# Performance work log

Hardware: AMD Instinct MI355X
Metric: run time of the kernel (lower is better)

The kernel has to match this reference:

```python
import jax, jax.numpy as jnp
from jax import lax
import numpy as np
from jax.scipy.special import logsumexp

B, T, K = 64, 4096, 32

def setup_inputs() -> dict:
    key = jax.random.key(0)
    k1, k2, k3 = jax.random.split(key, 3)
    return {
        "emission_logp": jax.random.normal(k1, (B, T, K), dtype=jnp.float32),
        "log_pi": jax.random.normal(k2, (K,), dtype=jnp.float32),
        "log_A": jax.random.normal(k3, (K, K), dtype=jnp.float32),
    }

def reference(emission_logp, log_pi, log_A):
    b, t, k = emission_logp.shape
    lp = jax.nn.log_softmax(log_pi)            # [K]
    lA = jax.nn.log_softmax(log_A, axis=1)     # [K,K]
    em = jnp.swapaxes(emission_logp, 0, 1)     # [T,B,K] time-major for scan

    # forward recursion: alpha_t = logsumexp_i(alpha_{t-1,i} + A_{i,j}) + em_t
    a0 = lp[None, :] + em[0]                   # [B,K]
    def fstep(a_prev, e_t):
        a_new = logsumexp(a_prev[:, :, None] + lA[None, :, :], axis=1) + e_t
        return a_new, a_new
    _, alphas = lax.scan(fstep, a0, em[1:])
    alpha = jnp.concatenate([a0[None], alphas], axis=0)  # [T,B,K]

    # backward recursion: beta_t = logsumexp_j(beta_{t+1,j} + A_{i,j} + em_{t+1,j})
    bT = jnp.zeros((b, k), dtype=emission_logp.dtype)
    def bstep(b_next, e_next):
        b_new = logsumexp(b_next[:, None, :] + lA[None, :, :] + e_next[:, None, :], axis=2)
        return b_new, b_new
    _, betas = lax.scan(bstep, bT, em[1:], reverse=True)
    beta = jnp.concatenate([betas, bT[None]], axis=0)    # [T,B,K]

    log_gamma = alpha + beta
    log_gamma = log_gamma - logsumexp(log_gamma, axis=-1, keepdims=True)
    return jnp.swapaxes(log_gamma, 0, 1)       # [B,T,K]
```

## Files before the change

kernel.cpp:

```cpp
#include <hip/hip_runtime.h>

#define B_ 64
#define T_ 4096
#define K_ 32
#define C_ 128
#define L_ 32
#define W_ 32
#define NPH 16

typedef float f32x16 __attribute__((ext_vector_type(16)));
typedef float f32x4v __attribute__((ext_vector_type(4)));
typedef short s16x8 __attribute__((ext_vector_type(8)));

union W4 { unsigned u[4]; short s[8]; s16x8 v; };

__device__ __forceinline__ unsigned cvt_pk_bf16(float lo, float hi) {
  unsigned r;
  asm("v_cvt_pk_bf16_f32 %0, %1, %2" : "=v"(r) : "v"(lo), "v"(hi));
  return r;
}
__device__ __forceinline__ short f2bf(float x) {
  unsigned u = __float_as_uint(x);
  return (short)((u + 0x7FFFu + ((u >> 16) & 1u)) >> 16);
}
__device__ __forceinline__ float wmax32(float v) {
#pragma unroll
  for (int k = 16; k >= 1; k >>= 1) v = fmaxf(v, __shfl_xor(v, k, 32));
  return v;
}
__device__ __forceinline__ float wsum32(float v) {
#pragma unroll
  for (int k = 16; k >= 1; k >>= 1) v += __shfl_xor(v, k, 32);
  return v;
}

__global__ __launch_bounds__(256) void pet_kernel(const float* __restrict__ em,
                                                  const float* __restrict__ log_pi,
                                                  const float* __restrict__ log_A,
                                                  float* __restrict__ eA,
                                                  float* __restrict__ lp,
                                                  unsigned* __restrict__ peP) {
  const int bid = (int)blockIdx.x;
  const int tid = (int)threadIdx.x;
  if (bid >= T_) {
    const int i0 = tid >> 5, j = tid & 31;
#pragma unroll
    for (int rr = 0; rr < 4; ++rr) {
      int i = i0 + 8 * rr;
      float a = log_A[i * K_ + j];
      float m = wmax32(a);
      float e = __expf(a - m);
      float S = wsum32(e);
      eA[i * K_ + j] = e / S;
    }
    if (i0 == 0) {
      float v = log_pi[j];
      float m2 = wmax32(v);
      float ee = __expf(v - m2);
      float SS = wsum32(ee);
      lp[j] = v - m2 - __logf(SS);
    }
    return;
  }
  const int t = ((bid & 7) << 9) + (bid >> 3);
  __shared__ float tile[K_][B_];
  const int b = tid >> 2, kq = tid & 3;
  const float* p = em + (size_t)b * (T_ * K_) + (size_t)t * K_ + kq * 8;
  f32x4v v0 = *(const f32x4v*)p;
  f32x4v v1 = *(const f32x4v*)(p + 4);
#pragma unroll
  for (int q = 0; q < 4; ++q) tile[kq * 8 + q][b] = __expf(v0[q]);
#pragma unroll
  for (int q = 0; q < 4; ++q) tile[kq * 8 + 4 + q][b] = __expf(v1[q]);
  __syncthreads();
  unsigned* ob = peP + (size_t)t * 1024;
#pragma unroll
  for (int rr = 0; rr < 4; ++rr) {
    int Wd = tid + 256 * rr;
    int col = Wd & 63, wq = (Wd >> 6) & 7, hh = Wd >> 9;
    int s0 = 2 * (wq & 1) + 8 * (wq >> 1) + 4 * hh;
    ob[Wd] = cvt_pk_bf16(tile[s0][col], tile[s0 + 1][col]);
  }
}

__global__ __launch_bounds__(256) void hmm_kernel(const unsigned* __restrict__ peP,
                                                  const float* __restrict__ eA,
                                                  const float* __restrict__ lp,
                                                  float* __restrict__ out) {
  __shared__ __align__(16) unsigned aw[L_ * 512];
  __shared__ __align__(16) unsigned bw[L_ * 512];
  __shared__ __align__(16) unsigned prF[2 * 4 * 512];
  __shared__ __align__(16) unsigned prB[2 * 4 * 512];

  const int bid = (int)blockIdx.x;
  const int c = ((bid & 7) << 4) + ((bid >> 3) & 15);
  const int g = bid >> 7;
  const int tid = (int)threadIdx.x;
  const int wv = tid >> 6;
  const int l = tid & 63;
  const int h = l >> 5;
  const int m = l & 31;
  const int t0 = c * L_;

  const int dsgn = (wv == 3) ? -1 : 1;
  const int tbase = (wv == 3) ? (t0 + L_ - 1 + W_) : (t0 - W_);
  const unsigned* gsrc = peP + (g << 5) + ((l >> 3) << 6) + ((l & 7) << 2);
  uint4 pr[2][8];

  W4 A1u, A2u, B1u, B2u;
  unsigned rg[8];
  f32x16 zk;
#pragma unroll
  for (int r = 0; r < 16; ++r) zk[r] = 0.0f;

  if (wv < 2) {
#pragma unroll
    for (int r = 0; r < 8; ++r) {
      const int k1 = (r & 3) + 8 * (r >> 2) + 4 * h;
      const int k2 = k1 + 16;
      float a1 = (wv == 0) ? eA[k1 * K_ + m] : eA[m * K_ + k1];
      float a2 = (wv == 0) ? eA[k2 * K_ + m] : eA[m * K_ + k2];
      A1u.s[r] = f2bf(a1);
      A2u.s[r] = f2bf(a2);
    }
#pragma unroll
    for (int q = 0; q < 4; ++q) { B1u.u[q] = 0x3F803F80u; B2u.u[q] = 0x3F803F80u; }
  } else {
    unsigned* ring = (wv == 2) ? prF : prB;
#pragma unroll
    for (int i = 0; i < 8; ++i) {
      int tv = tbase + dsgn * (i >> 1);
      tv = tv < 0 ? 0 : (tv > T_ - 1 ? T_ - 1 : tv);
      pr[0][i] = *(const uint4*)(gsrc + (size_t)tv * 1024 + ((i & 1) << 9));
    }
#pragma unroll
    for (int i = 0; i < 8; ++i)
      *(uint4*)&ring[((i >> 1)) * 512 + ((i & 1) << 8) + 4 * l] = pr[0][i];
#pragma unroll
    for (int i = 0; i < 8; ++i) {
      int tv = tbase + dsgn * (4 + (i >> 1));
      tv = tv < 0 ? 0 : (tv > T_ - 1 ? T_ - 1 : tv);
      pr[1][i] = *(const uint4*)(gsrc + (size_t)tv * 1024 + ((i & 1) << 9));
    }
  }
  __syncthreads();

#define FSTEP(P, U)                                                            \
  {                                                                            \
    const int sg = 4 * (P) + (U);                                              \
    _Pragma("unroll") for (int w = 0; w < 8; ++w)                              \
      rg[w] = prF[(((P) & 1) * 4 + (U)) * 512 + h * 256 + w * 32 + m];         \
    f32x16 acc = __builtin_amdgcn_mfma_f32_32x32x16_bf16(A1u.v, B1u.v, zk, 0, 0, 0); \
    acc = __builtin_amdgcn_mfma_f32_32x32x16_bf16(A2u.v, B2u.v, acc, 0, 0, 0); \
    if (sg == 32 && c == 0) {                                                  \
      _Pragma("unroll") for (int r = 0; r < 16; ++r)                           \
        acc[r] = __expf(lp[(r & 3) + 8 * (r >> 2) + 4 * h]);                   \
    }                                                                          \
    float al[16];                                                              \
    _Pragma("unroll") for (int w = 0; w < 8; ++w) {                            \
      al[2 * w]     = acc[2 * w]     * __uint_as_float(rg[w] << 16);           \
      al[2 * w + 1] = acc[2 * w + 1] * __uint_as_float(rg[w] & 0xFFFF0000u);   \
    }                                                                          \
    if ((sg & 7) == 7) {                                                       \
      float a0 = __shfl(al[0], m, 64);                                         \
      float rs = __builtin_amdgcn_rcpf(a0);                                    \
      _Pragma("unroll") for (int r = 0; r < 16; ++r) al[r] *= rs;              \
    }                                                                          \
    W4 nB1, nB2;                                                               \
    _Pragma("unroll") for (int q = 0; q < 4; ++q) {                            \
      nB1.u[q] = cvt_pk_bf16(al[2 * q], al[2 * q + 1]);                        \
      nB2.u[q] = cvt_pk_bf16(al[8 + 2 * q], al[8 + 2 * q + 1]);                \
    }                                                                          \
    if (sg >= 32) {                                                            \
      unsigned* bp = &aw[(sg - 32) * 512 + ((h << 5) + m) * 8];                \
      *(uint4*)bp = *(uint4*)nB1.u;                                            \
      *(uint4*)(bp + 4) = *(uint4*)nB2.u;                                      \
    }                                                                          \
    B1u = nB1; B2u = nB2;                                                      \
  }

#define BSTEP(P, U)                                                            \
  {                                                                            \
    const int sg = 4 * (P) + (U);                                              \
    _Pragma("unroll") for (int w = 0; w < 8; ++w)                              \
      rg[w] = prB[(((P) & 1) * 4 + (U)) * 512 + h * 256 + w * 32 + m];         \
    f32x16 acc = __builtin_amdgcn_mfma_f32_32x32x16_bf16(A1u.v, B1u.v, zk, 0, 0, 0); \
    acc = __builtin_amdgcn_mfma_f32_32x32x16_bf16(A2u.v, B2u.v, acc, 0, 0, 0); \
    if (sg == 32 && c == C_ - 1) {                                             \
      _Pragma("unroll") for (int r = 0; r < 16; ++r) acc[r] = 1.0f;            \
    }                                                                          \
    if (sg >= 32) {                                                            \
      W4 s1, s2;                                                               \
      _Pragma("unroll") for (int q = 0; q < 4; ++q) {                          \
        s1.u[q] = cvt_pk_bf16(acc[2 * q], acc[2 * q + 1]);                     \
        s2.u[q] = cvt_pk_bf16(acc[8 + 2 * q], acc[8 + 2 * q + 1]);             \
      }                                                                        \
      unsigned* bp = &bw[(63 - sg) * 512 + ((h << 5) + m) * 8];                \
      *(uint4*)bp = *(uint4*)s1.u;                                             \
      *(uint4*)(bp + 4) = *(uint4*)s2.u;                                       \
    }                                                                          \
    float al[16];                                                              \
    _Pragma("unroll") for (int w = 0; w < 8; ++w) {                            \
      al[2 * w]     = acc[2 * w]     * __uint_as_float(rg[w] << 16);           \
      al[2 * w + 1] = acc[2 * w + 1] * __uint_as_float(rg[w] & 0xFFFF0000u);   \
    }                                                                          \
    if ((sg & 7) == 7) {                                                       \
      float a0 = __shfl(al[0], m, 64);                                         \
      float rs = __builtin_amdgcn_rcpf(a0);                                    \
      _Pragma("unroll") for (int r = 0; r < 16; ++r) al[r] *= rs;              \
    }                                                                          \
    W4 nB1, nB2;                                                               \
    _Pragma("unroll") for (int q = 0; q < 4; ++q) {                            \
      nB1.u[q] = cvt_pk_bf16(al[2 * q], al[2 * q + 1]);                        \
      nB2.u[q] = cvt_pk_bf16(al[8 + 2 * q], al[8 + 2 * q + 1]);                \
    }                                                                          \
    B1u = nB1; B2u = nB2;                                                      \
  }

#pragma unroll
  for (int p = 0; p < NPH; ++p) {
    if (wv == 0) {
      FSTEP(p, 0) FSTEP(p, 1) FSTEP(p, 2) FSTEP(p, 3)
    } else if (wv == 1) {
      BSTEP(p, 0) BSTEP(p, 1) BSTEP(p, 2) BSTEP(p, 3)
    } else {
      unsigned* ring = (wv == 2) ? prF : prB;
      if (p < NPH - 1) {
#pragma unroll
        for (int i = 0; i < 8; ++i)
          *(uint4*)&ring[(((p + 1) & 1) * 4 + (i >> 1)) * 512 + ((i & 1) << 8) + 4 * l] =
              pr[(p + 1) & 1][i];
      }
      if (p < NPH - 2) {
#pragma unroll
        for (int i = 0; i < 8; ++i) {
          int tv = tbase + dsgn * (4 * (p + 2) + (i >> 1));
          tv = tv < 0 ? 0 : (tv > T_ - 1 ? T_ - 1 : tv);
          pr[p & 1][i] = *(const uint4*)(gsrc + (size_t)tv * 1024 + ((i & 1) << 9));
        }
      }
    }
    __syncthreads();
  }

  {
#pragma unroll
    for (int rr = 0; rr < 8; ++rr) {
      const int row = wv * 8 + rr;
      const unsigned* ap = &aw[row * 512 + ((h << 5) + m) * 8];
      const unsigned* bp = &bw[row * 512 + ((h << 5) + m) * 8];
      uint4 a1 = *(const uint4*)ap, a2 = *(const uint4*)(ap + 4);
      uint4 b1 = *(const uint4*)bp, b2 = *(const uint4*)(bp + 4);
      float gg[16];
#pragma unroll
      for (int q = 0; q < 4; ++q) {
        unsigned ua = ((const unsigned*)&a1)[q], ub = ((const unsigned*)&b1)[q];
        gg[2 * q]     = __uint_as_float(ua << 16) * __uint_as_float(ub << 16);
        gg[2 * q + 1] = __uint_as_float(ua & 0xFFFF0000u) * __uint_as_float(ub & 0xFFFF0000u);
        unsigned va = ((const unsigned*)&a2)[q], vb = ((const unsigned*)&b2)[q];
        gg[8 + 2 * q]     = __uint_as_float(va << 16) * __uint_as_float(vb << 16);
        gg[8 + 2 * q + 1] = __uint_as_float(va & 0xFFFF0000u) * __uint_as_float(vb & 0xFFFF0000u);
      }
      float s = 0.0f;
#pragma unroll
      for (int r = 0; r < 16; ++r) s += gg[r];
      s += __shfl_xor(s, 32, 64);
      const float ls = __log2f(s);
      float* po = out + (size_t)((g << 5) + m) * (T_ * K_) + (size_t)(t0 + row) * K_;
#pragma unroll
      for (int w = 0; w < 8; ++w) {
        const int k0 = 2 * (w & 1) + 8 * (w >> 1) + 4 * h;
        float2 v;
        v.x = (__log2f(gg[2 * w]) - ls) * 0.6931471805599453f;
        v.y = (__log2f(gg[2 * w + 1]) - ls) * 0.6931471805599453f;
        *(float2*)(po + k0) = v;
      }
    }
  }
}

extern "C" void kernel_launch(void* const* d_in, const int* in_sizes, int n_in,
                              void* d_out, int out_size, void* d_ws, size_t ws_size,
                              hipStream_t stream) {
  const float* em = (const float*)d_in[0];
  const float* log_pi = (const float*)d_in[1];
  const float* log_A = (const float*)d_in[2];
  float* out = (float*)d_out;

  float* eA = (float*)d_ws;
  float* lp = eA + K_ * K_;
  unsigned* peP = (unsigned*)((char*)d_ws + 8192);

  pet_kernel<<<T_ + 1, 256, 0, stream>>>(em, log_pi, log_A, eA, lp, peP);
  hmm_kernel<<<2 * C_, 256, 0, stream>>>(peP, eA, lp, out);
}
```

Baseline: 41.79 us.

## Use shorter chunks with more blocks and per-lane register prefetch rings

Splits the time axis into 512 chunks of 8 steps with a 28-step warmup, in place of 128 chunks of 32 steps with a 32-step warmup. Each block now has two waves and no dedicated loader waves. Each compute wave prefetches its emission columns four steps ahead into registers, which removes the per-phase __syncthreads and the LDS staging ring. The shared-memory layout of the alpha and beta buffers changes to scalar strided stores. This gives more parallelism and a shorter serial chain per block, but the warmup-to-output ratio rises from 1:1 to 3.5:1, so redundant work grows and loads use narrower scalar accesses.

```diff
diff --git a/kernel.cpp b/kernel.cpp
--- a/kernel.cpp
+++ b/kernel.cpp
@@ -3,10 +3,11 @@
 #define B_ 64
 #define T_ 4096
 #define K_ 32
-#define C_ 128
-#define L_ 32
-#define W_ 32
-#define NPH 16
+#define C_ 512
+#define L_ 8
+#define W_ 28
+#define PFD 4
+#define NS (W_ + L_)
 
 typedef float f32x16 __attribute__((ext_vector_type(16)));
 typedef float f32x4v __attribute__((ext_vector_type(4)));
@@ -83,76 +84,67 @@
   }
 }
 
-__global__ __launch_bounds__(256) void hmm_kernel(const unsigned* __restrict__ peP,
-                                                  const float* __restrict__ eA,
-                                                  const float* __restrict__ lp,
-                                                  float* __restrict__ out) {
+__global__ __launch_bounds__(128) void hmm2_kernel(const unsigned* __restrict__ peP,
+                                                   const float* __restrict__ eA,
+                                                   const float* __restrict__ lp,
+                                                   float* __restrict__ out) {
   __shared__ __align__(16) unsigned aw[L_ * 512];
   __shared__ __align__(16) unsigned bw[L_ * 512];
-  __shared__ __align__(16) unsigned prF[2 * 4 * 512];
-  __shared__ __align__(16) unsigned prB[2 * 4 * 512];
-
   const int bid = (int)blockIdx.x;
-  const int c = ((bid & 7) << 4) + ((bid >> 3) & 15);
-  const int g = bid >> 7;
+  const int c = ((bid & 7) << 6) + ((bid >> 3) & 63);
+  const int g = bid >> 9;
   const int tid = (int)threadIdx.x;
   const int wv = tid >> 6;
   const int l = tid & 63;
   const int h = l >> 5;
   const int m = l & 31;
   const int t0 = c * L_;
-
-  const int dsgn = (wv == 3) ? -1 : 1;
-  const int tbase = (wv == 3) ? (t0 + L_ - 1 + W_) : (t0 - W_);
-  const unsigned* gsrc = peP + (g << 5) + ((l >> 3) << 6) + ((l & 7) << 2);
-  uint4 pr[2][8];
+  const unsigned* pB = peP + (h << 9) + (g << 5) + m;
+
+  f32x16 zk;
+#pragma unroll
+  for (int r = 0; r < 16; ++r) zk[r] = 0.0f;
 
   W4 A1u, A2u, B1u, B2u;
-  unsigned rg[8];
-  f32x16 zk;
-#pragma unroll
-  for (int r = 0; r < 16; ++r) zk[r] = 0.0f;
-
-  if (wv < 2) {
-#pragma unroll
-    for (int r = 0; r < 8; ++r) {
-      const int k1 = (r & 3) + 8 * (r >> 2) + 4 * h;
-      const int k2 = k1 + 16;
-      float a1 = (wv == 0) ? eA[k1 * K_ + m] : eA[m * K_ + k1];
-      float a2 = (wv == 0) ? eA[k2 * K_ + m] : eA[m * K_ + k2];
-      A1u.s[r] = f2bf(a1);
-      A2u.s[r] = f2bf(a2);
-    }
-#pragma unroll
-    for (int q = 0; q < 4; ++q) { B1u.u[q] = 0x3F803F80u; B2u.u[q] = 0x3F803F80u; }
+#pragma unroll
+  for (int r = 0; r < 8; ++r) {
+    const int k1 = (r & 3) + 8 * (r >> 2) + 4 * h;
+    const int k2 = k1 + 16;
+    float a1 = (wv == 0) ? eA[k1 * K_ + m] : eA[m * K_ + k1];
+    float a2 = (wv == 0) ? eA[k2 * K_ + m] : eA[m * K_ + k2];
+    A1u.s[r] = f2bf(a1);
+    A2u.s[r] = f2bf(a2);
+  }
+#pragma unroll
+  for (int q = 0; q < 4; ++q) { B1u.u[q] = 0x3F803F80u; B2u.u[q] = 0x3F803F80u; }
+
+  unsigned ring[PFD][8];
+  if (wv == 0) {
+#pragma unroll
+    for (int u = 0; u < PFD; ++u) {
+      int tt = t0 - W_ + u; if (tt < 0) tt = 0;
+      const unsigned* pp = pB + (size_t)tt * 1024;
+#pragma unroll
+      for (int w = 0; w < 8; ++w) ring[u][w] = pp[w * 64];
+    }
   } else {
-    unsigned* ring = (wv == 2) ? prF : prB;
-#pragma unroll
-    for (int i = 0; i < 8; ++i) {
-      int tv = tbase + dsgn * (i >> 1);
-      tv = tv < 0 ? 0 : (tv > T_ - 1 ? T_ - 1 : tv);
-      pr[0][i] = *(const uint4*)(gsrc + (size_t)tv * 1024 + ((i & 1) << 9));
-    }
-#pragma unroll
-    for (int i = 0; i < 8; ++i)
-      *(uint4*)&ring[((i >> 1)) * 512 + ((i & 1) << 8) + 4 * l] = pr[0][i];
-#pragma unroll
-    for (int i = 0; i < 8; ++i) {
-      int tv = tbase + dsgn * (4 + (i >> 1));
-      tv = tv < 0 ? 0 : (tv > T_ - 1 ? T_ - 1 : tv);
-      pr[1][i] = *(const uint4*)(gsrc + (size_t)tv * 1024 + ((i & 1) << 9));
-    }
-  }
-  __syncthreads();
-
-#define FSTEP(P, U)                                                            \
+#pragma unroll
+    for (int u = 0; u < PFD; ++u) {
+      int tt = t0 + L_ - 1 + W_ - u; if (tt > T_ - 1) tt = T_ - 1;
+      const unsigned* pp = pB + (size_t)tt * 1024;
+#pragma unroll
+      for (int w = 0; w < 8; ++w) ring[u][w] = pp[w * 64];
+    }
+  }
+
+#define FSTEP(S)                                                               \
   {                                                                            \
-    const int sg = 4 * (P) + (U);                                              \
-    _Pragma("unroll") for (int w = 0; w < 8; ++w)                              \
-      rg[w] = prF[(((P) & 1) * 4 + (U)) * 512 + h * 256 + w * 32 + m];         \
+    const int t = t0 + ((S) - W_);                                             \
+    unsigned rg[8];                                                            \
+    _Pragma("unroll") for (int w = 0; w < 8; ++w) rg[w] = ring[(S) & 3][w];    \
     f32x16 acc = __builtin_amdgcn_mfma_f32_32x32x16_bf16(A1u.v, B1u.v, zk, 0, 0, 0); \
     acc = __builtin_amdgcn_mfma_f32_32x32x16_bf16(A2u.v, B2u.v, acc, 0, 0, 0); \
-    if (sg == 32 && c == 0) {                                                  \
+    if (t == 0) {             \
       _Pragma("unroll") for (int r = 0; r < 16; ++r)                           \
         acc[r] = __expf(lp[(r & 3) + 8 * (r >> 2) + 4 * h]);                   \
     }                                                                          \
@@ -161,7 +153,10 @@
       al[2 * w]     = acc[2 * w]     * __uint_as_float(rg[w] << 16);           \
       al[2 * w + 1] = acc[2 * w + 1] * __uint_as_float(rg[w] & 0xFFFF0000u);   \
     }                                                                          \
-    if ((sg & 7) == 7) {                                                       \
+    { int tn = t + PFD; if (tn < 0) tn = 0; if (tn > T_ - 1) tn = T_ - 1;      \
+      const unsigned* pp = pB + (size_t)tn * 1024;                             \
+      _Pragma("unroll") for (int w = 0; w < 8; ++w) ring[(S) & 3][w] = pp[w * 64]; } \
+    if (((S) & 7) == 7) {                                                      \
       float a0 = __shfl(al[0], m, 64);                                         \
       float rs = __builtin_amdgcn_rcpf(a0);                                    \
       _Pragma("unroll") for (int r = 0; r < 16; ++r) al[r] *= rs;              \
@@ -171,40 +166,47 @@
       nB1.u[q] = cvt_pk_bf16(al[2 * q], al[2 * q + 1]);                        \
       nB2.u[q] = cvt_pk_bf16(al[8 + 2 * q], al[8 + 2 * q + 1]);                \
     }                                                                          \
-    if (sg >= 32) {                                                            \
-      unsigned* bp = &aw[(sg - 32) * 512 + ((h << 5) + m) * 8];                \
-      *(uint4*)bp = *(uint4*)nB1.u;                                            \
-      *(uint4*)(bp + 4) = *(uint4*)nB2.u;                                      \
+    if ((S) >= W_) {                                                           \
+      unsigned* bp = &aw[(((S) - W_) << 9) + h * 32 + m];                      \
+      _Pragma("unroll") for (int q = 0; q < 4; ++q) {                          \
+        bp[q * 64] = nB1.u[q];                                                 \
+        bp[(4 + q) * 64] = nB2.u[q];                                           \
+      }                                                                        \
     }                                                                          \
     B1u = nB1; B2u = nB2;                                                      \
   }
 
-#define BSTEP(P, U)                                                            \
+#define BSTEP(S)                                                               \
   {                                                                            \
-    const int sg = 4 * (P) + (U);                                              \
-    _Pragma("unroll") for (int w = 0; w < 8; ++w)                              \
-      rg[w] = prB[(((P) & 1) * 4 + (U)) * 512 + h * 256 + w * 32 + m];         \
+    const int t = t0 + (L_ - 1 + W_ - (S));                                    \
+    unsigned rg[8];                                                            \
+    _Pragma("unroll") for (int w = 0; w < 8; ++w) rg[w] = ring[(S) & 3][w];    \
     f32x16 acc = __builtin_amdgcn_mfma_f32_32x32x16_bf16(A1u.v, B1u.v, zk, 0, 0, 0); \
     acc = __builtin_amdgcn_mfma_f32_32x32x16_bf16(A2u.v, B2u.v, acc, 0, 0, 0); \
-    if (sg == 32 && c == C_ - 1) {                                             \
+    if (t == T_ - 1) {                         \
       _Pragma("unroll") for (int r = 0; r < 16; ++r) acc[r] = 1.0f;            \
     }                                                                          \
-    if (sg >= 32) {                                                            \
+    if ((S) >= W_) {                                                           \
       W4 s1, s2;                                                               \
       _Pragma("unroll") for (int q = 0; q < 4; ++q) {                          \
         s1.u[q] = cvt_pk_bf16(acc[2 * q], acc[2 * q + 1]);                     \
         s2.u[q] = cvt_pk_bf16(acc[8 + 2 * q], acc[8 + 2 * q + 1]);             \
       }                                                                        \
-      unsigned* bp = &bw[(63 - sg) * 512 + ((h << 5) + m) * 8];                \
-      *(uint4*)bp = *(uint4*)s1.u;                                             \
-      *(uint4*)(bp + 4) = *(uint4*)s2.u;                                       \
+      unsigned* bp = &bw[((L_ - 1 + W_ - (S)) << 9) + h * 32 + m];             \
+      _Pragma("unroll") for (int q = 0; q < 4; ++q) {                          \
+        bp[q * 64] = s1.u[q];                                                  \
+        bp[(4 + q) * 64] = s2.u[q];                                            \
+      }                                                                        \
     }                                                                          \
     float al[16];                                                              \
     _Pragma("unroll") for (int w = 0; w < 8; ++w) {                            \
       al[2 * w]     = acc[2 * w]     * __uint_as_float(rg[w] << 16);           \
       al[2 * w + 1] = acc[2 * w + 1] * __uint_as_float(rg[w] & 0xFFFF0000u);   \
     }                                                                          \
-    if ((sg & 7) == 7) {                                                       \
+    { int tn = t - PFD; if (tn < 0) tn = 0; if (tn > T_ - 1) tn = T_ - 1;      \
+      const unsigned* pp = pB + (size_t)tn * 1024;                             \
+      _Pragma("unroll") for (int w = 0; w < 8; ++w) ring[(S) & 3][w] = pp[w * 64]; } \
+    if (((S) & 7) == 7) {                                                      \
       float a0 = __shfl(al[0], m, 64);                                         \
       float rs = __builtin_amdgcn_rcpf(a0);                                    \
       _Pragma("unroll") for (int r = 0; r < 16; ++r) al[r] *= rs;              \
@@ -217,51 +219,31 @@
     B1u = nB1; B2u = nB2;                                                      \
   }
 
-#pragma unroll
-  for (int p = 0; p < NPH; ++p) {
-    if (wv == 0) {
-      FSTEP(p, 0) FSTEP(p, 1) FSTEP(p, 2) FSTEP(p, 3)
-    } else if (wv == 1) {
-      BSTEP(p, 0) BSTEP(p, 1) BSTEP(p, 2) BSTEP(p, 3)
-    } else {
-      unsigned* ring = (wv == 2) ? prF : prB;
-      if (p < NPH - 1) {
-#pragma unroll
-        for (int i = 0; i < 8; ++i)
-          *(uint4*)&ring[(((p + 1) & 1) * 4 + (i >> 1)) * 512 + ((i & 1) << 8) + 4 * l] =
-              pr[(p + 1) & 1][i];
+#define REP4F(B) FSTEP(B) FSTEP((B) + 1) FSTEP((B) + 2) FSTEP((B) + 3)
+#define REP4B(B) BSTEP(B) BSTEP((B) + 1) BSTEP((B) + 2) BSTEP((B) + 3)
+
+  if (wv == 0) {
+    REP4F(0) REP4F(4) REP4F(8) REP4F(12) REP4F(16) REP4F(20) REP4F(24) REP4F(28) REP4F(32)
+  } else {
+    REP4B(0) REP4B(4) REP4B(8) REP4B(12) REP4B(16) REP4B(20) REP4B(24) REP4B(28) REP4B(32)
+  }
+
+  __syncthreads();
+
+  {
+#pragma unroll
+    for (int rr = 0; rr < 4; ++rr) {
+      const int row = (wv << 2) + rr;
+      const unsigned* pa = aw + (row << 9) + (h << 5) + m;
+      const unsigned* pb = bw + (row << 9) + (h << 5) + m;
+      float gg[16];
+      float s = 0.0f;
+#pragma unroll
+      for (int w = 0; w < 8; ++w) {
+        unsigned ua = pa[w * 64], ub = pb[w * 64];
+        gg[2 * w]     = __uint_as_float(ua << 16) * __uint_as_float(ub << 16);
+        gg[2 * w + 1] = __uint_as_float(ua & 0xFFFF0000u) * __uint_as_float(ub & 0xFFFF0000u);
       }
-      if (p < NPH - 2) {
-#pragma unroll
-        for (int i = 0; i < 8; ++i) {
-          int tv = tbase + dsgn * (4 * (p + 2) + (i >> 1));
-          tv = tv < 0 ? 0 : (tv > T_ - 1 ? T_ - 1 : tv);
-          pr[p & 1][i] = *(const uint4*)(gsrc + (size_t)tv * 1024 + ((i & 1) << 9));
-        }
-      }
-    }
-    __syncthreads();
-  }
-
-  {
-#pragma unroll
-    for (int rr = 0; rr < 8; ++rr) {
-      const int row = wv * 8 + rr;
-      const unsigned* ap = &aw[row * 512 + ((h << 5) + m) * 8];
-      const unsigned* bp = &bw[row * 512 + ((h << 5) + m) * 8];
-      uint4 a1 = *(const uint4*)ap, a2 = *(const uint4*)(ap + 4);
-      uint4 b1 = *(const uint4*)bp, b2 = *(const uint4*)(bp + 4);
-      float gg[16];
-#pragma unroll
-      for (int q = 0; q < 4; ++q) {
-        unsigned ua = ((const unsigned*)&a1)[q], ub = ((const unsigned*)&b1)[q];
-        gg[2 * q]     = __uint_as_float(ua << 16) * __uint_as_float(ub << 16);
-        gg[2 * q + 1] = __uint_as_float(ua & 0xFFFF0000u) * __uint_as_float(ub & 0xFFFF0000u);
-        unsigned va = ((const unsigned*)&a2)[q], vb = ((const unsigned*)&b2)[q];
-        gg[8 + 2 * q]     = __uint_as_float(va << 16) * __uint_as_float(vb << 16);
-        gg[8 + 2 * q + 1] = __uint_as_float(va & 0xFFFF0000u) * __uint_as_float(vb & 0xFFFF0000u);
-      }
-      float s = 0.0f;
 #pragma unroll
       for (int r = 0; r < 16; ++r) s += gg[r];
       s += __shfl_xor(s, 32, 64);
@@ -292,5 +274,5 @@
   unsigned* peP = (unsigned*)((char*)d_ws + 8192);
 
   pet_kernel<<<T_ + 1, 256, 0, stream>>>(em, log_pi, log_A, eA, lp, peP);
-  hmm_kernel<<<2 * C_, 256, 0, stream>>>(peP, eA, lp, out);
-}
+  hmm2_kernel<<<2 * C_, 128, 0, stream>>>(peP, eA, lp, out);
+}
```

Measured after the change: 35.80 us. -14.3%, faster.
